# Kernel tuning notes

Measured on AMD Instinct MI355X. Metric: run time of the kernel, lower is better.

The kernel has to match this reference:

```python
import jax, jax.numpy as jnp
import numpy as np

TEMPERATURE = 0.1
NEG_INF = -9e15

def setup_inputs() -> dict:
    key = jax.random.key(0)
    k1, k2 = jax.random.split(key)
    B, D = 4096, 256
    z_i = jax.random.normal(k1, (B, D), dtype=jnp.float32)
    z_j = jax.random.normal(k2, (B, D), dtype=jnp.float32)
    return {"z_i": z_i, "z_j": z_j}

def _l2norm(x, eps=1e-12):
    # matches F.normalize(dim=1): x / max(||x||, eps)
    n = jnp.sqrt(jnp.sum(x * x, axis=1, keepdims=True))
    return x / jnp.maximum(n, eps)

def reference(z_i, z_j):
    B = z_i.shape[0]
    zi = _l2norm(z_i)
    zj = _l2norm(z_j)
    reps = jnp.concatenate([zi, zj], axis=0)  # [2B, D], unit rows
    # cosine similarity of unit vectors == dot product
    sim = reps @ reps.T  # [2B, 2B]
    N = 2 * B
    eye = jnp.eye(N, dtype=bool)
    sim = jnp.where(eye, NEG_INF, sim)
    # positives: offset +B and -B diagonals
    pos = jnp.concatenate([sim[jnp.arange(B), jnp.arange(B) + B],
                           sim[jnp.arange(B) + B, jnp.arange(B)]], axis=0)  # [2B]
    pos = pos / TEMPERATURE
    sim = sim / TEMPERATURE
    denom = jnp.sum(jnp.exp(sim), axis=1)  # [2B]
    loss = -jnp.mean(pos - jnp.log(denom))
    return loss
```

## Files before the change

kernel.cpp:

```cpp
#include <hip/hip_runtime.h>
#include <hip/hip_bf16.h>
#include <stdint.h>

#define NROWS 8192
#define BROWS 4096
#define LN2 0.6931471805599453f
#define FSC 8.944507e-4f
#define KMAD 7503
#define CBITS 1064989150
#define NBLK 2112

typedef __attribute__((ext_vector_type(4))) int i32x4;

__device__ inline void gload_lds16(const void* g, void* l) {
  __builtin_amdgcn_global_load_lds((const __attribute__((address_space(1))) void*)g,
                                   (__attribute__((address_space(3))) void*)l,
                                   16, 0, 0);
}

__device__ inline int cum_blocks(int it) {
  int n = 132 - it, m = n >> 2, r = n & 3;
  return NBLK - (2 * m * (m - 1) + r * m);
}

__global__ __launch_bounds__(256) void knorm(const float* __restrict__ zi,
                                             const float* __restrict__ zj,
                                             int* __restrict__ reps,
                                             int* __restrict__ qss,
                                             float* __restrict__ denom,
                                             float* __restrict__ out) {
  int w = threadIdx.x >> 6, l = threadIdx.x & 63;
  int row = blockIdx.x * 4 + w;
  const float* src = (row < BROWS) ? (zi + (size_t)row * 256)
                                   : (zj + (size_t)(row - BROWS) * 256);
  float4 v = ((const float4*)src)[l];
  float ss = v.x * v.x + v.y * v.y + v.z * v.z + v.w * v.w;
#pragma unroll
  for (int m = 1; m < 64; m <<= 1) ss += __shfl_xor(ss, m, 64);
  float sc = 127.0f / fmaxf(sqrtf(ss), 1e-12f);
  int q0 = __float2int_rn(v.x * sc), q1 = __float2int_rn(v.y * sc);
  int q2 = __float2int_rn(v.z * sc), q3 = __float2int_rn(v.w * sc);
  reps[(size_t)row * 64 + l] =
      (q0 & 255) | ((q1 & 255) << 8) | ((q2 & 255) << 16) | ((q3 & 255) << 24);
  int qs = q0 * q0 + q1 * q1 + q2 * q2 + q3 * q3;
#pragma unroll
  for (int m = 1; m < 64; m <<= 1) qs += __shfl_xor(qs, m, 64);
  if (l == 0) { denom[row] = 0.f; qss[row] = qs; }
  if (row == 0 && l == 0) out[0] = 0.f;
}

__global__ __launch_bounds__(64, 2) void ksim(const int* __restrict__ reps_,
                                              float* __restrict__ denom,
                                              float* __restrict__ pos) {
  __shared__ uint4 smem[2][512];
  __shared__ float colacc[256];
  int l = threadIdx.x;
  int kgrp = l >> 4;

  int b = blockIdx.x;
  int orig = (b & 7) * 264 + (b >> 3);
  float f = 8.0f * (float)(NBLK - orig) + 0.25f;
  int it = 132 - (int)(sqrtf(f) + 0.5f);
  if (it < 0) it = 0;
  if (it > 127) it = 127;
  while (it < 127 && cum_blocks(it + 1) <= orig) ++it;
  while (it > 0 && cum_blocks(it) > orig) --it;
  int q = orig - cum_blocks(it);
  int rowbase = it * 64;
  int cs0 = rowbase + q * 256;
  int len = NROWS - cs0; if (len > 256) len = 256;
  int ntile = len >> 5;

#pragma unroll
  for (int i = 0; i < 4; ++i) colacc[l + 64 * i] = 0.f;

  auto stage = [&](int bufi, int colbase) {
#pragma unroll
    for (int i = 0; i < 8; ++i) {
      int lr = i * 4 + (l >> 4);
      int kb = ((l & 15) * 16) ^ ((lr & 15) << 4);
      gload_lds16((const char*)reps_ + (size_t)(colbase + lr) * 256 + kb,
                  (void*)&smem[bufi][i * 64]);
    }
  };
  stage(0, cs0);

  i32x4 a[4][4];
  {
    const uint4* r4 = (const uint4*)reps_;
    int arow = rowbase + (l & 15);
#pragma unroll
    for (int fr = 0; fr < 4; ++fr)
#pragma unroll
      for (int kk = 0; kk < 4; ++kk)
        a[fr][kk] = __builtin_bit_cast(i32x4,
            r4[(size_t)(arow + fr * 16) * 16 + kk * 4 + kgrp]);
  }

  float rowsum[4][4];
#pragma unroll
  for (int fr = 0; fr < 4; ++fr)
#pragma unroll
    for (int r = 0; r < 4; ++r) rowsum[fr][r] = 0.f;

  int r0 = rowbase + kgrp * 4;
  int buf = 0;
  const int kmad = KMAD;
  const int cbits = CBITS;

  for (int t = 0; t < ntile; ++t) {
    bool hasNext = (t + 1 < ntile);
    if (hasNext) stage(buf ^ 1, cs0 + 32 * (t + 1));

    const char* bb = (const char*)&smem[0][0] + buf * 8192;
    i32x4 acc[4][2];
    const i32x4 zero = {0, 0, 0, 0};

    auto half = [&](int fc) {
      __builtin_amdgcn_s_setprio(1);
#pragma unroll
      for (int kk = 0; kk < 4; ++kk) {
        int lr = (l & 15) + fc * 16;
        i32x4 bf = *(const i32x4*)(bb + lr * 256 + ((((kk * 4 + kgrp) ^ (lr & 15))) << 4));
#pragma unroll
        for (int fr = 0; fr < 4; ++fr) {
          if (kk == 0)
            acc[fr][fc] = __builtin_amdgcn_mfma_i32_16x16x64_i8(a[fr][0], bf, zero, 0, 0, 0);
          else
            acc[fr][fc] = __builtin_amdgcn_mfma_i32_16x16x64_i8(a[fr][kk], bf, acc[fr][fc], 0, 0, 0);
        }
      }
      __builtin_amdgcn_s_setprio(0);
    };

    if (t == 0) {
      asm volatile("s_waitcnt vmcnt(8)" ::: "memory");
      __builtin_amdgcn_sched_barrier(0);
      half(0); half(1);
    } else if (hasNext) {
      asm volatile("s_waitcnt vmcnt(12)" ::: "memory");
      __builtin_amdgcn_sched_barrier(0);
      half(0);
      asm volatile("s_waitcnt vmcnt(8)" ::: "memory");
      __builtin_amdgcn_sched_barrier(0);
      half(1);
    } else {
      asm volatile("s_waitcnt vmcnt(4)" ::: "memory");
      __builtin_amdgcn_sched_barrier(0);
      half(0);
      asm volatile("s_waitcnt vmcnt(0)" ::: "memory");
      __builtin_amdgcn_sched_barrier(0);
      half(1);
    }

    int cb = cs0 + 32 * t;
    bool docol = !(q == 0 && t < 2);
    bool dopos = (q == 16) && (t < 2);
    float cp0 = 0.f, cp1 = 0.f;
#pragma unroll
    for (int fr = 0; fr < 4; ++fr)
#pragma unroll
      for (int fc = 0; fc < 2; ++fc)
#pragma unroll
        for (int r = 0; r < 4; ++r) {
          int I = acc[fr][fc][r];
          int ib;
          asm("v_mad_i32_i24 %0, %1, %2, %3"
              : "=v"(ib) : "v"(I), "s"(kmad), "v"(cbits));
          float e = __builtin_bit_cast(float, ib);
          if (dopos) {
            int rg = r0 + fr * 16 + r;
            int cg = cb + (l & 15) + fc * 16;
            if (cg == rg + BROWS) pos[rg] = (float)I * FSC;
          }
          rowsum[fr][r] += e;
          if (fc == 0) cp0 += e; else cp1 += e;
        }
    if (docol) {
      cp0 += __shfl_xor(cp0, 16, 64); cp0 += __shfl_xor(cp0, 32, 64);
      cp1 += __shfl_xor(cp1, 16, 64); cp1 += __shfl_xor(cp1, 32, 64);
      if (l < 16) {
        int off = (cb - cs0) + l;
        colacc[off] += cp0;
        colacc[off + 16] += cp1;
      }
    }
    buf ^= 1;
  }

#pragma unroll
  for (int fr = 0; fr < 4; ++fr)
#pragma unroll
    for (int r = 0; r < 4; ++r) {
      float vv = rowsum[fr][r];
      vv += __shfl_xor(vv, 1, 64);
      vv += __shfl_xor(vv, 2, 64);
      vv += __shfl_xor(vv, 4, 64);
      vv += __shfl_xor(vv, 8, 64);
      if ((l & 15) == 0) atomicAdd(&denom[r0 + fr * 16 + r], vv);
    }

#pragma unroll
  for (int i = 0; i < 4; ++i) {
    int off = l + 64 * i;
    float vv = colacc[off];
    if (vv != 0.f) atomicAdd(&denom[cs0 + off], vv);
  }
}

__global__ __launch_bounds__(256) void kfin(const float* __restrict__ denom,
                                            const float* __restrict__ pos,
                                            const int* __restrict__ qss,
                                            float* __restrict__ out) {
  int i = blockIdx.x * 256 + threadIdx.x;
  int ib = qss[i] * KMAD + CBITS;
  float diag_e = __builtin_bit_cast(float, ib);
  float v = (logf(denom[i] - diag_e) - pos[i & 4095] * LN2) * (1.0f / 8192.0f);
#pragma unroll
  for (int m = 1; m < 64; m <<= 1) v += __shfl_xor(v, m, 64);
  __shared__ float part[4];
  if ((threadIdx.x & 63) == 0) part[threadIdx.x >> 6] = v;
  __syncthreads();
  if (threadIdx.x == 0)
    atomicAdd(out, part[0] + part[1] + part[2] + part[3]);
}

extern "C" void kernel_launch(void* const* d_in, const int* in_sizes, int n_in,
                              void* d_out, int out_size, void* d_ws, size_t ws_size,
                              hipStream_t stream) {
  (void)in_sizes; (void)n_in; (void)out_size; (void)ws_size;
  const float* zi = (const float*)d_in[0];
  const float* zj = (const float*)d_in[1];
  float* out = (float*)d_out;
  char* ws = (char*)d_ws;
  int* reps    = (int*)ws;
  float* denom = (float*)(ws + 2097152);
  float* pos   = (float*)(ws + 2097152 + 32768);
  int* qss     = (int*)(ws + 2097152 + 32768 + 16384);

  knorm<<<2048, 256, 0, stream>>>(zi, zj, reps, qss, denom, out);
  ksim<<<NBLK, 64, 0, stream>>>(reps, denom, pos);
  kfin<<<32, 256, 0, stream>>>(denom, pos, qss, out);
}
```

Measured before the change: 37.91 us.

## Load B tiles directly into double-buffered registers instead of LDS staging

Drops the global_load_lds staging of column tiles through double-buffered shared memory. Each lane now loads its MFMA B fragments straight from global memory into two register buffers, alternating between them across tiles. The intent is to cut LDS traffic, the LDS reads and the LDS footprint, which may also allow more resident blocks. The cost is higher VGPR pressure and less coalesced 16-byte global loads per lane spread across rows.

```diff
diff --git a/kernel.cpp b/kernel.cpp
--- a/kernel.cpp
+++ b/kernel.cpp
@@ -11,12 +11,6 @@
 #define NBLK 2112
 
 typedef __attribute__((ext_vector_type(4))) int i32x4;
-
-__device__ inline void gload_lds16(const void* g, void* l) {
-  __builtin_amdgcn_global_load_lds((const __attribute__((address_space(1))) void*)g,
-                                   (__attribute__((address_space(3))) void*)l,
-                                   16, 0, 0);
-}
 
 __device__ inline int cum_blocks(int it) {
   int n = 132 - it, m = n >> 2, r = n & 3;
@@ -52,7 +46,6 @@
 __global__ __launch_bounds__(64, 2) void ksim(const int* __restrict__ reps_,
                                               float* __restrict__ denom,
                                               float* __restrict__ pos) {
-  __shared__ uint4 smem[2][512];
   __shared__ float colacc[256];
   int l = threadIdx.x;
   int kgrp = l >> 4;
@@ -74,20 +67,10 @@
 #pragma unroll
   for (int i = 0; i < 4; ++i) colacc[l + 64 * i] = 0.f;
 
-  auto stage = [&](int bufi, int colbase) {
-#pragma unroll
-    for (int i = 0; i < 8; ++i) {
-      int lr = i * 4 + (l >> 4);
-      int kb = ((l & 15) * 16) ^ ((lr & 15) << 4);
-      gload_lds16((const char*)reps_ + (size_t)(colbase + lr) * 256 + kb,
-                  (void*)&smem[bufi][i * 64]);
-    }
-  };
-  stage(0, cs0);
+  const uint4* r4 = (const uint4*)reps_;
 
   i32x4 a[4][4];
   {
-    const uint4* r4 = (const uint4*)reps_;
     int arow = rowbase + (l & 15);
 #pragma unroll
     for (int fr = 0; fr < 4; ++fr)
@@ -97,6 +80,18 @@
             r4[(size_t)(arow + fr * 16) * 16 + kk * 4 + kgrp]);
   }
 
+  auto loadB = [&](i32x4 (&dst)[8], int cb) {
+    const uint4* bp = r4 + (size_t)(cb + (l & 15)) * 16 + kgrp;
+#pragma unroll
+    for (int kk = 0; kk < 4; ++kk) {
+      dst[kk]     = __builtin_bit_cast(i32x4, bp[kk * 4]);
+      dst[kk + 4] = __builtin_bit_cast(i32x4, bp[kk * 4 + 256]);
+    }
+  };
+
+  i32x4 bfA[8], bfB[8];
+  loadB(bfA, cs0);
+
   float rowsum[4][4];
 #pragma unroll
   for (int fr = 0; fr < 4; ++fr)
@@ -104,54 +99,30 @@
     for (int r = 0; r < 4; ++r) rowsum[fr][r] = 0.f;
 
   int r0 = rowbase + kgrp * 4;
-  int buf = 0;
   const int kmad = KMAD;
   const int cbits = CBITS;
 
-  for (int t = 0; t < ntile; ++t) {
-    bool hasNext = (t + 1 < ntile);
-    if (hasNext) stage(buf ^ 1, cs0 + 32 * (t + 1));
-
-    const char* bb = (const char*)&smem[0][0] + buf * 8192;
+  auto step = [&](i32x4 (&cur)[8], int t, bool lastWait) {
+    if (lastWait) asm volatile("s_waitcnt vmcnt(0)" ::: "memory");
+    else          asm volatile("s_waitcnt vmcnt(8)" ::: "memory");
+    __builtin_amdgcn_sched_barrier(0);
+
     i32x4 acc[4][2];
     const i32x4 zero = {0, 0, 0, 0};
-
-    auto half = [&](int fc) {
-      __builtin_amdgcn_s_setprio(1);
-#pragma unroll
-      for (int kk = 0; kk < 4; ++kk) {
-        int lr = (l & 15) + fc * 16;
-        i32x4 bf = *(const i32x4*)(bb + lr * 256 + ((((kk * 4 + kgrp) ^ (lr & 15))) << 4));
-#pragma unroll
-        for (int fr = 0; fr < 4; ++fr) {
-          if (kk == 0)
-            acc[fr][fc] = __builtin_amdgcn_mfma_i32_16x16x64_i8(a[fr][0], bf, zero, 0, 0, 0);
-          else
-            acc[fr][fc] = __builtin_amdgcn_mfma_i32_16x16x64_i8(a[fr][kk], bf, acc[fr][fc], 0, 0, 0);
+    __builtin_amdgcn_s_setprio(1);
+#pragma unroll
+    for (int kk = 0; kk < 4; ++kk)
+#pragma unroll
+      for (int fr = 0; fr < 4; ++fr) {
+        if (kk == 0) {
+          acc[fr][0] = __builtin_amdgcn_mfma_i32_16x16x64_i8(a[fr][0], cur[0], zero, 0, 0, 0);
+          acc[fr][1] = __builtin_amdgcn_mfma_i32_16x16x64_i8(a[fr][0], cur[4], zero, 0, 0, 0);
+        } else {
+          acc[fr][0] = __builtin_amdgcn_mfma_i32_16x16x64_i8(a[fr][kk], cur[kk], acc[fr][0], 0, 0, 0);
+          acc[fr][1] = __builtin_amdgcn_mfma_i32_16x16x64_i8(a[fr][kk], cur[kk + 4], acc[fr][1], 0, 0, 0);
         }
       }
-      __builtin_amdgcn_s_setprio(0);
-    };
-
-    if (t == 0) {
-      asm volatile("s_waitcnt vmcnt(8)" ::: "memory");
-      __builtin_amdgcn_sched_barrier(0);
-      half(0); half(1);
-    } else if (hasNext) {
-      asm volatile("s_waitcnt vmcnt(12)" ::: "memory");
-      __builtin_amdgcn_sched_barrier(0);
-      half(0);
-      asm volatile("s_waitcnt vmcnt(8)" ::: "memory");
-      __builtin_amdgcn_sched_barrier(0);
-      half(1);
-    } else {
-      asm volatile("s_waitcnt vmcnt(4)" ::: "memory");
-      __builtin_amdgcn_sched_barrier(0);
-      half(0);
-      asm volatile("s_waitcnt vmcnt(0)" ::: "memory");
-      __builtin_amdgcn_sched_barrier(0);
-      half(1);
-    }
+    __builtin_amdgcn_s_setprio(0);
 
     int cb = cs0 + 32 * t;
     bool docol = !(q == 0 && t < 2);
@@ -185,7 +156,13 @@
         colacc[off + 16] += cp1;
       }
     }
-    buf ^= 1;
+  };
+
+  for (int t = 0; t < ntile; t += 2) {
+    if (t + 1 < ntile) loadB(bfB, cs0 + 32 * (t + 1));
+    step(bfA, t, t + 1 >= ntile);
+    if (t + 2 < ntile) loadB(bfA, cs0 + 32 * (t + 2));
+    step(bfB, t + 1, t + 2 >= ntile);
   }
 
 #pragma unroll
```

Measured after the change: 49.81 us. 1.31x slower.
